# Kernel optimization log

Hardware: AMD Instinct MI355X
Metric: run time of the kernel (lower is better)

Reference implementation:

```python
import jax, jax.numpy as jnp
import numpy as np

N_SPK, N_UTT, D = 1024, 32, 128
EPS = 1e-8  # matches F.cosine_similarity eps


def setup_inputs() -> dict:
    key = jax.random.key(0)
    emb = jax.random.normal(key, (N_SPK * N_UTT, D), dtype=jnp.float32)
    emb = emb / jnp.linalg.norm(emb, axis=-1, keepdims=True)  # L2-normalized per docstring
    return {
        "embeddings": emb,
        "w": jnp.asarray(10.0, dtype=jnp.float32),
        "b": jnp.asarray(-5.0, dtype=jnp.float32),
        "n_speakers": N_SPK,
        "n_utterances": N_UTT,
    }


def reference(embeddings, w, b, n_speakers, n_utterances):
    # [N, M, D]
    e = embeddings.reshape(n_speakers, n_utterances, -1)
    cent = e.mean(axis=1)  # [N, D] full centroids
    # exclusive centroids: mean over all utterances except i -> [N, M, D]
    cent_excl = (e.sum(axis=1, keepdims=True) - e) / (n_utterances - 1)

    e_n = jnp.maximum(jnp.linalg.norm(e, axis=-1), EPS)          # [N, M]
    c_n = jnp.maximum(jnp.linalg.norm(cent, axis=-1), EPS)       # [N]
    ce_n = jnp.maximum(jnp.linalg.norm(cent_excl, axis=-1), EPS) # [N, M]

    # cosine sim of every utterance vs every full centroid: [N, M, N]
    sim = jnp.einsum('nmd,kd->nmk', e, cent) / (e_n[:, :, None] * c_n[None, None, :])
    # own-speaker entry uses the exclusive centroid instead
    sim_own = jnp.sum(e * cent_excl, axis=-1) / (e_n * ce_n)     # [N, M]
    eye = jnp.eye(n_speakers, dtype=bool)[:, None, :]            # [N, 1, N]
    sim = jnp.where(eye, sim_own[:, :, None], sim)

    logits = (w * sim + b).reshape(n_speakers * n_utterances, n_speakers)
    targets = jnp.repeat(jnp.arange(n_speakers), n_utterances)
    logp = jax.nn.log_softmax(logits, axis=-1)
    loss = -jnp.take_along_axis(logp, targets[:, None], axis=-1).mean()
    return loss
```

## Files before the change

kernel.cpp:

```cpp
#include <hip/hip_runtime.h>
#include <math.h>

#define NSPK 1024
#define NUTT 32
#define DIM  128
#define NROWS (NSPK * NUTT)
#define EPS 1e-8f
#define LOG2E 1.44269504f

typedef __attribute__((ext_vector_type(8))) short short8;
typedef __attribute__((ext_vector_type(4))) float floatx4;

__device__ inline unsigned short f2bf(float f) {
  union { float f; unsigned u; } v; v.f = f;
  unsigned r = v.u + 0x7fffu + ((v.u >> 16) & 1u);
  return (unsigned short)(r >> 16);
}

__device__ __forceinline__ void gll16(const unsigned short* g, unsigned short* l) {
  __builtin_amdgcn_global_load_lds(
      (const __attribute__((address_space(1))) unsigned int*)g,
      (__attribute__((address_space(3))) unsigned int*)l, 16, 0, 0);
}

__global__ __launch_bounds__(256) void k1(const float* __restrict__ emb,
                                          const float* __restrict__ wp,
                                          const float* __restrict__ bp,
                                          unsigned short* __restrict__ centC,
                                          float* __restrict__ rs2g,
                                          float* __restrict__ eolg,
                                          float* __restrict__ olvg,
                                          float* __restrict__ out) {
  __shared__ __align__(16) float Sl[2 * 128];
  __shared__ float red[4];

  int b = blockIdx.x, t = threadIdx.x;
  float w = wp[0], bb = bp[0];
  float M = bb + fabsf(w);
  if (b == 0 && t == 0) out[0] = 0.f;

  int sp = t >> 7, d = t & 127;
  {
    const float* eb = emb + (size_t)(b * 2 + sp) * NUTT * DIM + d;
    float s = 0.f;
#pragma unroll
    for (int m = 0; m < NUTT; ++m) s += eb[m * DIM];
    Sl[sp * 128 + d] = s;
    float p = s * s;
#pragma unroll
    for (int mask = 1; mask < 64; mask <<= 1) p += __shfl_xor(p, mask, 64);
    if ((t & 63) == 0) red[t >> 6] = p;
  }
  __syncthreads();
  float ss0 = red[0] + red[1], ss1 = red[2] + red[3];

  {
    float ss = sp ? ss1 : ss0;
    float s = Sl[sp * 128 + d];
    float cn = fmaxf(sqrtf(ss) * (1.0f / NUTT), EPS);
    centC[(size_t)(d >> 3) * (NSPK * 8) + (size_t)(b * 2 + sp) * 8 + (d & 7)] =
        f2bf(s / (NUTT * cn));
  }

  {
    int row = t >> 2, sub = t & 3;
    int rsp = row >> 5;
    const float* er = emb + (size_t)(b * 64 + row) * DIM + sub * 32;
    const float* Srow = &Sl[rsp * 128 + sub * 32];
    float ee = 0.f, es = 0.f;
#pragma unroll
    for (int i = 0; i < 8; ++i) {
      float4 ev = *(const float4*)&er[i * 4];
      float4 sv = *(const float4*)&Srow[i * 4];
      ee += ev.x * ev.x + ev.y * ev.y + ev.z * ev.z + ev.w * ev.w;
      es += ev.x * sv.x + ev.y * sv.y + ev.z * sv.z + ev.w * sv.w;
    }
    ee += __shfl_xor(ee, 1, 64); es += __shfl_xor(es, 1, 64);
    ee += __shfl_xor(ee, 2, 64); es += __shfl_xor(es, 2, 64);
    if (sub == 0) {
      float ss = rsp ? ss1 : ss0;
      float en = fmaxf(sqrtf(ee), EPS);
      float dot_own = (es - ee) * (1.0f / (NUTT - 1));
      float ex2 = (ss - 2.f * es + ee) * (1.0f / ((NUTT - 1) * (NUTT - 1)));
      float cen = fmaxf(sqrtf(ex2), EPS);
      float ol = w * dot_own / (en * cen) + bb;
      int gr = b * 64 + row;
      olvg[gr] = ol;
      eolg[gr] = exp2f((ol - M) * LOG2E);
      rs2g[gr] = w * LOG2E / en;
    }
  }
}

__global__ __launch_bounds__(256, 2) void k2(const float* __restrict__ emb,
                                             const unsigned short* __restrict__ centC,
                                             const float* __restrict__ rs2g,
                                             const float* __restrict__ eolg,
                                             const float* __restrict__ olvg,
                                             const float* __restrict__ wp,
                                             const float* __restrict__ bp,
                                             float* __restrict__ out) {
  __shared__ __align__(16) unsigned short A[64 * 136];
  __shared__ __align__(16) unsigned short Bb[2][8192];
  __shared__ __align__(16) float sPart[256];

  int b = blockIdx.x, t = threadIdx.x;
  int wid = t >> 6, lane = t & 63, lg = lane >> 4, lc = lane & 15;
  float w = wp[0], bb = bp[0];
  float M = bb + fabsf(w);
  float c2 = -fabsf(w) * LOG2E;

#pragma unroll
  for (int i = 0; i < 8; ++i) {
    int idx4 = t + 256 * i;
    int r = idx4 >> 5, d4 = (idx4 & 31) << 2;
    float4 v = *(const float4*)(emb + (size_t)b * 8192 + (size_t)idx4 * 4);
    ushort4 bv;
    bv.x = f2bf(v.x); bv.y = f2bf(v.y); bv.z = f2bf(v.z); bv.w = f2bf(v.w);
    *(ushort4*)&A[r * 136 + d4] = bv;
  }

  const unsigned short* gbase = centC + ((size_t)(wid * 4 + lg) * NSPK + lc) * 8;
  {
#pragma unroll
    for (int i = 0; i < 4; ++i)
      gll16(gbase + (size_t)i * 16 * 8, &Bb[0][i * 2048 + wid * 512]);
  }

  __syncthreads();

  short8 af[4][4];
#pragma unroll
  for (int rt = 0; rt < 4; ++rt)
#pragma unroll
    for (int ks = 0; ks < 4; ++ks)
      af[rt][ks] = *(const short8*)&A[(rt * 16 + lc) * 136 + ks * 32 + lg * 8];

  float rsL[16], eolL[16];
#pragma unroll
  for (int rt = 0; rt < 4; ++rt) {
    float4 r4 = *(const float4*)&rs2g[b * 64 + rt * 16 + lg * 4];
    float4 o4 = *(const float4*)&eolg[b * 64 + rt * 16 + lg * 4];
    rsL[rt * 4 + 0] = r4.x; rsL[rt * 4 + 1] = r4.y; rsL[rt * 4 + 2] = r4.z; rsL[rt * 4 + 3] = r4.w;
    eolL[rt * 4 + 0] = o4.x; eolL[rt * 4 + 1] = o4.y; eolL[rt * 4 + 2] = o4.z; eolL[rt * 4 + 3] = o4.w;
  }

  float sAcc[16];
#pragma unroll
  for (int j = 0; j < 16; ++j) sAcc[j] = 0.f;

  for (int p = 0; p < 16; ++p) {
    if (p > 0) __syncthreads();
    if (p < 15) {
      const unsigned short* gp = gbase + (size_t)(p + 1) * 64 * 8;
      unsigned short* lb = Bb[(p + 1) & 1];
#pragma unroll
      for (int i = 0; i < 4; ++i)
        gll16(gp + (size_t)i * 16 * 8, &lb[i * 2048 + wid * 512]);
    }

    const unsigned short* Bp = Bb[p & 1];
    short8 bf[4];
#pragma unroll
    for (int ks = 0; ks < 4; ++ks)
      bf[ks] = *(const short8*)&Bp[wid * 2048 + ks * 512 + lane * 8];

    floatx4 acc[4];
#pragma unroll
    for (int rt = 0; rt < 4; ++rt) acc[rt] = (floatx4){0.f, 0.f, 0.f, 0.f};
#pragma unroll
    for (int ks = 0; ks < 4; ++ks)
#pragma unroll
      for (int rt = 0; rt < 4; ++rt)
        acc[rt] = __builtin_amdgcn_mfma_f32_16x16x32_bf16(af[rt][ks], bf[ks], acc[rt], 0, 0, 0);

    int col = p * 64 + wid * 16 + lc;
#pragma unroll
    for (int rt = 0; rt < 4; ++rt) {
      int own = b * 2 + (rt >> 1);
      bool isown = (col == own);
#pragma unroll
      for (int reg = 0; reg < 4; ++reg) {
        float l2 = fmaf(rsL[rt * 4 + reg], acc[rt][reg], c2);
        float e = exp2f(l2);
        if (isown) e = eolL[rt * 4 + reg];
        sAcc[rt * 4 + reg] += e;
      }
    }
  }

#pragma unroll
  for (int mask = 1; mask < 16; mask <<= 1)
#pragma unroll
    for (int j = 0; j < 16; ++j) sAcc[j] += __shfl_xor(sAcc[j], mask, 64);

  if (lc == 0)
#pragma unroll
    for (int rt = 0; rt < 4; ++rt)
#pragma unroll
      for (int reg = 0; reg < 4; ++reg)
        sPart[wid * 64 + rt * 16 + lg * 4 + reg] = sAcc[rt * 4 + reg];
  __syncthreads();

  if (t < 64) {
    float st = sPart[t] + sPart[64 + t] + sPart[128 + t] + sPart[192 + t];
    float lossr = M + logf(st) - olvg[b * 64 + t];
#pragma unroll
    for (int mask = 1; mask < 64; mask <<= 1) lossr += __shfl_xor(lossr, mask, 64);
    if (t == 0) atomicAdd(out, lossr * (1.0f / NROWS));
  }
}

extern "C" void kernel_launch(void* const* d_in, const int* in_sizes, int n_in,
                              void* d_out, int out_size, void* d_ws, size_t ws_size,
                              hipStream_t stream) {
  const float* emb = (const float*)d_in[0];
  const float* wp  = (const float*)d_in[1];
  const float* bp  = (const float*)d_in[2];

  char* ws = (char*)d_ws;
  unsigned short* centC = (unsigned short*)ws;
  float* rs2g = (float*)(ws + 262144);
  float* eolg = (float*)(ws + 262144 + 131072);
  float* olvg = (float*)(ws + 262144 + 262144);
  float* out = (float*)d_out;

  hipLaunchKernelGGL(k1, dim3(512), dim3(256), 0, stream,
                     emb, wp, bp, centC, rs2g, eolg, olvg, out);
  hipLaunchKernelGGL(k2, dim3(512), dim3(256), 0, stream,
                     emb, centC, rs2g, eolg, olvg, wp, bp, out);
}
```

Baseline: 95.30 us.

## Split k2 work over eight waves with row-half/column-group tiling and MFMA-ordered LDS layout

Doubles k2's block size to 512 threads so each wave handles half the rows (2 row tiles instead of 4) for one 16-column group. This halves per-wave register use for A fragments and accumulators and adds latency hiding. The A tile in LDS is rewritten in a fragment-ordered layout with no padding, and the centroid tile loads are spread across the eight waves. In exchange, each wave issues the B-fragment LDS reads for less MFMA work, and block-wide barriers now span more waves.

```diff
diff --git a/kernel.cpp b/kernel.cpp
--- a/kernel.cpp
+++ b/kernel.cpp
@@ -92,7 +92,7 @@
   }
 }
 
-__global__ __launch_bounds__(256, 2) void k2(const float* __restrict__ emb,
+__global__ __launch_bounds__(512, 4) void k2(const float* __restrict__ emb,
                                              const unsigned short* __restrict__ centC,
                                              const float* __restrict__ rs2g,
                                              const float* __restrict__ eolg,
@@ -100,85 +100,94 @@
                                              const float* __restrict__ wp,
                                              const float* __restrict__ bp,
                                              float* __restrict__ out) {
-  __shared__ __align__(16) unsigned short A[64 * 136];
+  __shared__ __align__(16) unsigned short A[8192];
   __shared__ __align__(16) unsigned short Bb[2][8192];
-  __shared__ __align__(16) float sPart[256];
+  __shared__ __align__(16) float sPart[4][64];
 
   int b = blockIdx.x, t = threadIdx.x;
   int wid = t >> 6, lane = t & 63, lg = lane >> 4, lc = lane & 15;
+  int rh = wid & 1, cg = wid >> 1;
   float w = wp[0], bb = bp[0];
   float M = bb + fabsf(w);
   float c2 = -fabsf(w) * LOG2E;
 
 #pragma unroll
-  for (int i = 0; i < 8; ++i) {
-    int idx4 = t + 256 * i;
-    int r = idx4 >> 5, d4 = (idx4 & 31) << 2;
+  for (int i = 0; i < 4; ++i) {
+    int idx4 = t + 512 * i;
+    int row = idx4 >> 5, d4 = (idx4 & 31) << 2;
     float4 v = *(const float4*)(emb + (size_t)b * 8192 + (size_t)idx4 * 4);
     ushort4 bv;
     bv.x = f2bf(v.x); bv.y = f2bf(v.y); bv.z = f2bf(v.z); bv.w = f2bf(v.w);
-    *(ushort4*)&A[r * 136 + d4] = bv;
-  }
-
-  const unsigned short* gbase = centC + ((size_t)(wid * 4 + lg) * NSPK + lc) * 8;
-  {
-#pragma unroll
-    for (int i = 0; i < 4; ++i)
-      gll16(gbase + (size_t)i * 16 * 8, &Bb[0][i * 2048 + wid * 512]);
+    int rb = row >> 4, lcA = row & 15, kc = d4 >> 3, half = (d4 >> 2) & 1;
+    *(ushort4*)&A[(rb * 256 + kc * 16 + lcA) * 8 + half * 4] = bv;
+  }
+
+  {
+    int region = wid >> 1;
+#pragma unroll
+    for (int i = 0; i < 2; ++i) {
+      int ks = (wid & 1) * 2 + i;
+      gll16(centC + ((size_t)(ks * 4 + lg) * NSPK + region * 16 + lc) * 8,
+            &Bb[0][(region * 4 + ks) * 512]);
+    }
   }
 
   __syncthreads();
 
-  short8 af[4][4];
-#pragma unroll
-  for (int rt = 0; rt < 4; ++rt)
+  short8 af[2][4];
+#pragma unroll
+  for (int rt = 0; rt < 2; ++rt)
 #pragma unroll
     for (int ks = 0; ks < 4; ++ks)
-      af[rt][ks] = *(const short8*)&A[(rt * 16 + lc) * 136 + ks * 32 + lg * 8];
-
-  float rsL[16], eolL[16];
-#pragma unroll
-  for (int rt = 0; rt < 4; ++rt) {
-    float4 r4 = *(const float4*)&rs2g[b * 64 + rt * 16 + lg * 4];
-    float4 o4 = *(const float4*)&eolg[b * 64 + rt * 16 + lg * 4];
+      af[rt][ks] = *(const short8*)&A[((rh * 2 + rt) * 256 + (ks * 4 + lg) * 16 + lc) * 8];
+
+  float rsL[8], eolL[8];
+#pragma unroll
+  for (int rt = 0; rt < 2; ++rt) {
+    float4 r4 = *(const float4*)&rs2g[b * 64 + rh * 32 + rt * 16 + lg * 4];
+    float4 o4 = *(const float4*)&eolg[b * 64 + rh * 32 + rt * 16 + lg * 4];
     rsL[rt * 4 + 0] = r4.x; rsL[rt * 4 + 1] = r4.y; rsL[rt * 4 + 2] = r4.z; rsL[rt * 4 + 3] = r4.w;
     eolL[rt * 4 + 0] = o4.x; eolL[rt * 4 + 1] = o4.y; eolL[rt * 4 + 2] = o4.z; eolL[rt * 4 + 3] = o4.w;
   }
 
-  float sAcc[16];
-#pragma unroll
-  for (int j = 0; j < 16; ++j) sAcc[j] = 0.f;
+  float sAcc[8];
+#pragma unroll
+  for (int j = 0; j < 8; ++j) sAcc[j] = 0.f;
+
+  int own = b * 2 + rh;
 
   for (int p = 0; p < 16; ++p) {
     if (p > 0) __syncthreads();
     if (p < 15) {
-      const unsigned short* gp = gbase + (size_t)(p + 1) * 64 * 8;
+      int region = wid >> 1;
       unsigned short* lb = Bb[(p + 1) & 1];
 #pragma unroll
-      for (int i = 0; i < 4; ++i)
-        gll16(gp + (size_t)i * 16 * 8, &lb[i * 2048 + wid * 512]);
+      for (int i = 0; i < 2; ++i) {
+        int ks = (wid & 1) * 2 + i;
+        gll16(centC + ((size_t)(ks * 4 + lg) * NSPK + (p + 1) * 64 + region * 16 + lc) * 8,
+              &lb[(region * 4 + ks) * 512]);
+      }
     }
 
     const unsigned short* Bp = Bb[p & 1];
     short8 bf[4];
 #pragma unroll
     for (int ks = 0; ks < 4; ++ks)
-      bf[ks] = *(const short8*)&Bp[wid * 2048 + ks * 512 + lane * 8];
-
-    floatx4 acc[4];
-#pragma unroll
-    for (int rt = 0; rt < 4; ++rt) acc[rt] = (floatx4){0.f, 0.f, 0.f, 0.f};
+      bf[ks] = *(const short8*)&Bp[((cg * 4 + ks) * 64 + lane) * 8];
+
+    floatx4 acc[2];
+#pragma unroll
+    for (int rt = 0; rt < 2; ++rt) acc[rt] = (floatx4){0.f, 0.f, 0.f, 0.f};
 #pragma unroll
     for (int ks = 0; ks < 4; ++ks)
 #pragma unroll
-      for (int rt = 0; rt < 4; ++rt)
+      for (int rt = 0; rt < 2; ++rt)
         acc[rt] = __builtin_amdgcn_mfma_f32_16x16x32_bf16(af[rt][ks], bf[ks], acc[rt], 0, 0, 0);
 
-    int col = p * 64 + wid * 16 + lc;
-#pragma unroll
-    for (int rt = 0; rt < 4; ++rt) {
-      int own = b * 2 + (rt >> 1);
-      bool isown = (col == own);
+    int col = p * 64 + cg * 16 + lc;
+    bool isown = (col == own);
+#pragma unroll
+    for (int rt = 0; rt < 2; ++rt)
 #pragma unroll
       for (int reg = 0; reg < 4; ++reg) {
         float l2 = fmaf(rsL[rt * 4 + reg], acc[rt][reg], c2);
@@ -186,24 +195,23 @@
         if (isown) e = eolL[rt * 4 + reg];
         sAcc[rt * 4 + reg] += e;
       }
-    }
   }
 
 #pragma unroll
   for (int mask = 1; mask < 16; mask <<= 1)
 #pragma unroll
-    for (int j = 0; j < 16; ++j) sAcc[j] += __shfl_xor(sAcc[j], mask, 64);
+    for (int j = 0; j < 8; ++j) sAcc[j] += __shfl_xor(sAcc[j], mask, 64);
 
   if (lc == 0)
 #pragma unroll
-    for (int rt = 0; rt < 4; ++rt)
+    for (int rt = 0; rt < 2; ++rt)
 #pragma unroll
       for (int reg = 0; reg < 4; ++reg)
-        sPart[wid * 64 + rt * 16 + lg * 4 + reg] = sAcc[rt * 4 + reg];
+        sPart[cg][rh * 32 + rt * 16 + lg * 4 + reg] = sAcc[rt * 4 + reg];
   __syncthreads();
 
   if (t < 64) {
-    float st = sPart[t] + sPart[64 + t] + sPart[128 + t] + sPart[192 + t];
+    float st = sPart[0][t] + sPart[1][t] + sPart[2][t] + sPart[3][t];
     float lossr = M + logf(st) - olvg[b * 64 + t];
 #pragma unroll
     for (int mask = 1; mask < 64; mask <<= 1) lossr += __shfl_xor(lossr, mask, 64);
@@ -227,6 +235,6 @@
 
   hipLaunchKernelGGL(k1, dim3(512), dim3(256), 0, stream,
                      emb, wp, bp, centC, rs2g, eolg, olvg, out);
-  hipLaunchKernelGGL(k2, dim3(512), dim3(256), 0, stream,
+  hipLaunchKernelGGL(k2, dim3(512), dim3(512), 0, stream,
                      emb, centC, rs2g, eolg, olvg, wp, bp, out);
 }
```

After: 97.68 us. +2.5%, slower.
